# Optimization experiments

Hardware: AMD Instinct MI355X
Metric: run time of the kernel (lower is better)

Reference implementation:

```python
import jax, jax.numpy as jnp
import numpy as np

N_NODES = 100000
FEAT = 128
N_EDGES = 1600000


def setup_inputs() -> dict:
    key = jax.random.key(0)
    k1, k2, k3, k4, k5 = jax.random.split(key, 5)
    weight = jax.random.normal(k1, (N_NODES, FEAT), dtype=jnp.float32)
    cj = jax.random.uniform(k2, (N_NODES, 1), dtype=jnp.float32)
    ci = jax.random.uniform(k3, (N_NODES, 1), dtype=jnp.float32)
    src = jax.random.randint(k4, (N_EDGES,), 0, N_NODES, dtype=jnp.int32)
    dst = jax.random.randint(k5, (N_EDGES,), 0, N_NODES, dtype=jnp.int32)
    return {"weight": weight, "cj": cj, "ci": ci, "src": src, "dst": dst}


def reference(weight, cj, ci, src, dst):
    # feat = weight * dropout(cj); dropout_rate=0.0 -> identity
    feat = weight * cj                      # [N, F]
    msgs = feat[src]                        # [E, F] copy_src gather
    h = jax.ops.segment_sum(msgs, dst, num_segments=weight.shape[0])  # [N, F]
    return h * ci                           # dst-side normalize
```

## Files before the change

kernel.cpp:

```cpp
#include <hip/hip_runtime.h>
#include <hip/hip_bf16.h>

#define FEAT 128
#define BINW 128
#define BINSHIFT 7
#define MAXBIN 1024
#define CAP 4096
#define TB 8192

__device__ __forceinline__ unsigned short f2b(float f) {
    __hip_bfloat16 h = __float2bfloat16(f);
    return *reinterpret_cast<unsigned short*>(&h);
}
__device__ __forceinline__ float b2f_lo(unsigned u) {
    unsigned x = u << 16;
    float f;
    __builtin_memcpy(&f, &x, 4);
    return f;
}
__device__ __forceinline__ float b2f_hi(unsigned u) {
    unsigned x = u & 0xFFFF0000u;
    float f;
    __builtin_memcpy(&f, &x, 4);
    return f;
}
__device__ __forceinline__ unsigned int pack2(float lo, float hi) {
    return (unsigned int)f2b(lo) | ((unsigned int)f2b(hi) << 16);
}


__global__ void build_kernel(const float* __restrict__ weight,
                             const float* __restrict__ cj,
                             const int* __restrict__ src,
                             const int* __restrict__ dst,
                             unsigned short* __restrict__ feat16,
                             unsigned* __restrict__ pair,
                             int* __restrict__ binCursor,
                             int N, int E, int NBIN, int NTILE, int ipt) {
    __shared__ int h[MAXBIN];
    __shared__ int base_l[MAXBIN];
    int tile = blockIdx.x;

    int NC = N * (FEAT / 8);
    int cbase = tile * 256 * ipt;
    for (int j = 0; j < ipt; ++j) {
        int i = cbase + j * 256 + threadIdx.x;
        if (i < NC) {
            int row = i >> 4;
            int seg = i & 15;
            float c = cj[row];
            const float4* p = reinterpret_cast<const float4*>(
                weight + (size_t)row * FEAT + seg * 8);
            float4 a = p[0], b4 = p[1];
            uint4 o;
            o.x = pack2(a.x * c, a.y * c);
            o.y = pack2(a.z * c, a.w * c);
            o.z = pack2(b4.x * c, b4.y * c);
            o.w = pack2(b4.z * c, b4.w * c);
            *reinterpret_cast<uint4*>(feat16 + (size_t)i * 8) = o;
        }
    }

    if (tile >= NTILE) return;

    for (int b = threadIdx.x; b < NBIN; b += 256) h[b] = 0;
    __syncthreads();
    int e0 = tile * TB;
    #pragma unroll 4
    for (int i = 0; i < TB / 256; ++i) {
        int e = e0 + i * 256 + threadIdx.x;
        if (e < E) atomicAdd(&h[dst[e] >> BINSHIFT], 1);
    }
    __syncthreads();
    for (int b = threadIdx.x; b < NBIN; b += 256) {
        int c = h[b];
        int a = (c > 0) ? atomicAdd(&binCursor[b], c) : 0;
        base_l[b] = b * CAP + a;
        h[b] = 0;
    }
    __syncthreads();
    #pragma unroll 4
    for (int i = 0; i < TB / 256; ++i) {
        int e = e0 + i * 256 + threadIdx.x;
        if (e < E) {
            int d = dst[e];
            int b = d >> BINSHIFT;
            int pos = atomicAdd(&h[b], 1);
            int idx = base_l[b] + pos;
            if (idx < (b + 1) * CAP)
                pair[idx] = (unsigned)src[e] | ((unsigned)(d & (BINW - 1)) << 17);
        }
    }
}

__global__ void __launch_bounds__(512)
fine_sort_kernel(unsigned* __restrict__ pair,
                 const int* __restrict__ binCursor,
                 int2* __restrict__ nodeinfo,
                 int N) {
    __shared__ int cnt[BINW];
    __shared__ int sbase[BINW];
    __shared__ unsigned stage[CAP];
    int bin = blockIdx.x;
    int t = threadIdx.x;
    if (t < BINW) cnt[t] = 0;
    __syncthreads();
    int start = bin * CAP;
    int len = binCursor[bin];
    if (len > CAP) len = CAP;

    for (int k = t; k < len; k += 512) {
        unsigned p = pair[start + k];
        stage[k] = p;
        atomicAdd(&cnt[p >> 17], 1);
    }
    __syncthreads();
    int mine = (t < BINW) ? cnt[t] : 0;
    if (t < BINW) sbase[t] = mine;
    __syncthreads();
    for (int d = 1; d < BINW; d <<= 1) {
        int v = 0;
        if (t < BINW && t >= d) v = sbase[t - d];
        __syncthreads();
        if (t < BINW) sbase[t] += v;
        __syncthreads();
    }
    if (t < BINW) {
        int excl = sbase[t] - mine;
        int node = (bin << BINSHIFT) + t;
        if (node < N) nodeinfo[node] = make_int2(start + excl, mine);
        sbase[t] = start + excl;
        cnt[t] = 0;
    }
    __syncthreads();
    for (int k = t; k < len; k += 512) {
        unsigned p = stage[k];
        int ld = p >> 17;
        int pos = atomicAdd(&cnt[ld], 1);
        pair[sbase[ld] + pos] = p & 0x1FFFF;
    }
}

__global__ void gather_kernel(const unsigned short* __restrict__ feat16,
                              const float* __restrict__ ci,
                              const int2* __restrict__ nodeinfo,
                              const int* __restrict__ src_sorted,
                              float* __restrict__ out, int N) {
    int gt = blockIdx.x * blockDim.x + threadIdx.x;
    int node = gt >> 6;
    if (node >= N) return;
    int lane = gt & 63;
    int fi   = (lane & 15) << 3;
    int q    = lane >> 4;
    int2 ni  = nodeinfo[node];
    int start = ni.x;
    int end   = ni.x + ni.y;
    float acc[8] = {0.f, 0.f, 0.f, 0.f, 0.f, 0.f, 0.f, 0.f};
    #pragma unroll 4
    for (int k = start + q; k < end; k += 4) {
        int s = src_sorted[k];
        uint4 u = *reinterpret_cast<const uint4*>(feat16 + ((size_t)s << 7) + fi);
        acc[0] += b2f_lo(u.x); acc[1] += b2f_hi(u.x);
        acc[2] += b2f_lo(u.y); acc[3] += b2f_hi(u.y);
        acc[4] += b2f_lo(u.z); acc[5] += b2f_hi(u.z);
        acc[6] += b2f_lo(u.w); acc[7] += b2f_hi(u.w);
    }
    #pragma unroll
    for (int j = 0; j < 8; ++j) {
        acc[j] += __shfl_xor(acc[j], 16);
        acc[j] += __shfl_xor(acc[j], 32);
    }
    if (q == 0) {
        float c = ci[node];
        float4 v0 = make_float4(acc[0] * c, acc[1] * c, acc[2] * c, acc[3] * c);
        float4 v1 = make_float4(acc[4] * c, acc[5] * c, acc[6] * c, acc[7] * c);
        float* o = out + ((size_t)node << 7) + fi;
        *reinterpret_cast<float4*>(o)     = v0;
        *reinterpret_cast<float4*>(o + 4) = v1;
    }
}


__global__ void zero_ints_kernel(int* __restrict__ p, int n) {
    int i = blockIdx.x * blockDim.x + threadIdx.x;
    if (i < n) p[i] = 0;
}

__global__ void convert_hist_kernel(const float* __restrict__ weight,
                                    const float* __restrict__ cj,
                                    const int* __restrict__ dst,
                                    int* __restrict__ counts,
                                    unsigned short* __restrict__ feat16,
                                    int N, int E) {
    int i = blockIdx.x * blockDim.x + threadIdx.x;
    int NC = N * (FEAT / 8);
    if (i < NC) {
        int row = i >> 4;
        int seg = i & 15;
        float c = cj[row];
        const float4* p = reinterpret_cast<const float4*>(weight + (size_t)row * FEAT + seg * 8);
        float4 a = p[0], b = p[1];
        uint4 o;
        o.x = pack2(a.x * c, a.y * c);
        o.y = pack2(a.z * c, a.w * c);
        o.z = pack2(b.x * c, b.y * c);
        o.w = pack2(b.z * c, b.w * c);
        *reinterpret_cast<uint4*>(feat16 + (size_t)i * 8) = o;
    }
    if (i < E) atomicAdd(&counts[dst[i]], 1);
}

__global__ void block_sum_kernel(const int* __restrict__ counts, int* __restrict__ bsum, int N) {
    __shared__ int s[256];
    int i = blockIdx.x * 256 + threadIdx.x;
    s[threadIdx.x] = (i < N) ? counts[i] : 0;
    __syncthreads();
    for (int off = 128; off > 0; off >>= 1) {
        if (threadIdx.x < off) s[threadIdx.x] += s[threadIdx.x + off];
        __syncthreads();
    }
    if (threadIdx.x == 0) bsum[blockIdx.x] = s[0];
}

__global__ void scan_bsum_kernel(int* __restrict__ bsum, int nb) {
    __shared__ int s[512];
    int t = threadIdx.x;
    int mine = (t < nb) ? bsum[t] : 0;
    s[t] = mine;
    __syncthreads();
    for (int off = 1; off < 512; off <<= 1) {
        int v = (t >= off) ? s[t - off] : 0;
        __syncthreads();
        s[t] += v;
        __syncthreads();
    }
    if (t < nb) bsum[t] = s[t] - mine;
}

__global__ void scan_counts_kernel(const int* __restrict__ counts, const int* __restrict__ bsum,
                                   int* __restrict__ offsets, int* __restrict__ cursor,
                                   int N, int E) {
    __shared__ int s[256];
    int t = threadIdx.x;
    int i = blockIdx.x * 256 + t;
    int mine = (i < N) ? counts[i] : 0;
    s[t] = mine;
    __syncthreads();
    for (int off = 1; off < 256; off <<= 1) {
        int v = (t >= off) ? s[t - off] : 0;
        __syncthreads();
        s[t] += v;
        __syncthreads();
    }
    if (i < N) {
        int o = bsum[blockIdx.x] + s[t] - mine;
        offsets[i] = o;
        cursor[i] = o;
    }
    if (i == 0 && blockIdx.x == 0) offsets[N] = E;
}

__global__ void bucket_kernel(const int* __restrict__ src, const int* __restrict__ dst,
                              int* __restrict__ cursor,
                              int* __restrict__ src_sorted, int E) {
    int i = blockIdx.x * blockDim.x + threadIdx.x;
    if (i < E) {
        int pos = atomicAdd(&cursor[dst[i]], 1);
        src_sorted[pos] = src[i];
    }
}

__global__ void gather_mid_kernel(const unsigned short* __restrict__ feat16,
                                  const float* __restrict__ ci,
                                  const int* __restrict__ offsets,
                                  const int* __restrict__ src_sorted,
                                  float* __restrict__ out, int N) {
    int gt = blockIdx.x * blockDim.x + threadIdx.x;
    int node = gt >> 6;
    if (node >= N) return;
    int lane = gt & 63;
    int fi   = (lane & 15) << 3;
    int q    = lane >> 4;
    int start = offsets[node];
    int end   = offsets[node + 1];
    float acc[8] = {0.f, 0.f, 0.f, 0.f, 0.f, 0.f, 0.f, 0.f};
    #pragma unroll 4
    for (int k = start + q; k < end; k += 4) {
        int s = src_sorted[k];
        uint4 u = *reinterpret_cast<const uint4*>(feat16 + ((size_t)s << 7) + fi);
        acc[0] += b2f_lo(u.x); acc[1] += b2f_hi(u.x);
        acc[2] += b2f_lo(u.y); acc[3] += b2f_hi(u.y);
        acc[4] += b2f_lo(u.z); acc[5] += b2f_hi(u.z);
        acc[6] += b2f_lo(u.w); acc[7] += b2f_hi(u.w);
    }
    #pragma unroll
    for (int j = 0; j < 8; ++j) {
        acc[j] += __shfl_xor(acc[j], 16);
        acc[j] += __shfl_xor(acc[j], 32);
    }
    if (q == 0) {
        float c = ci[node];
        float4 v0 = make_float4(acc[0] * c, acc[1] * c, acc[2] * c, acc[3] * c);
        float4 v1 = make_float4(acc[4] * c, acc[5] * c, acc[6] * c, acc[7] * c);
        float* o = out + ((size_t)node << 7) + fi;
        *reinterpret_cast<float4*>(o)     = v0;
        *reinterpret_cast<float4*>(o + 4) = v1;
    }
}


__global__ void gcmc_zero_kernel(float4* __restrict__ out, int n4) {
    int i = blockIdx.x * blockDim.x + threadIdx.x;
    if (i < n4) out[i] = make_float4(0.f, 0.f, 0.f, 0.f);
}

__global__ void gcmc_scatter_kernel(const float* __restrict__ weight,
                                    const float* __restrict__ cj,
                                    const int* __restrict__ src,
                                    const int* __restrict__ dst,
                                    float* __restrict__ out,
                                    int n_edges) {
    int t = blockIdx.x * blockDim.x + threadIdx.x;
    int e = t >> 5;
    int f = (t & 31) << 2;
    if (e >= n_edges) return;
    int s = src[e];
    int d = dst[e];
    float c = cj[s];
    const float4 w = *reinterpret_cast<const float4*>(weight + (size_t)s * FEAT + f);
    float* o = out + (size_t)d * FEAT + f;
    unsafeAtomicAdd(o + 0, w.x * c);
    unsafeAtomicAdd(o + 1, w.y * c);
    unsafeAtomicAdd(o + 2, w.z * c);
    unsafeAtomicAdd(o + 3, w.w * c);
}

__global__ void gcmc_scale_kernel(float4* __restrict__ out,
                                  const float* __restrict__ ci, int n4) {
    int i = blockIdx.x * blockDim.x + threadIdx.x;
    if (i < n4) {
        float c = ci[i >> 5];
        float4 v = out[i];
        v.x *= c; v.y *= c; v.z *= c; v.w *= c;
        out[i] = v;
    }
}


static inline size_t align256(size_t x) { return (x + 255) & ~(size_t)255; }

extern "C" void kernel_launch(void* const* d_in, const int* in_sizes, int n_in,
                              void* d_out, int out_size, void* d_ws, size_t ws_size,
                              hipStream_t stream) {
    const float* weight = (const float*)d_in[0];
    const float* cj     = (const float*)d_in[1];
    const float* ci     = (const float*)d_in[2];
    const int*   src    = (const int*)d_in[3];
    const int*   dst    = (const int*)d_in[4];
    float* out = (float*)d_out;

    const int N = in_sizes[1];
    const int E = in_sizes[3];

    const int NBIN  = (N + BINW - 1) >> BINSHIFT;
    const int NTILE = (E + TB - 1) / TB;

    size_t o_feat = 0;
    size_t o_pair = align256(o_feat + (size_t)N * FEAT * 2);
    size_t o_cur  = align256(o_pair + (size_t)NBIN * CAP * 4);
    size_t o_ni   = align256(o_cur + (size_t)NBIN * 4);
    size_t need_new = o_ni + (size_t)N * 8;

    if (ws_size >= need_new && NBIN <= MAXBIN && N <= (1 << 17) &&
        (long)E <= (long)NBIN * (CAP / 2)) {
        char* ws = (char*)d_ws;
        unsigned short* feat16 = (unsigned short*)(ws + o_feat);
        unsigned* pair  = (unsigned*)(ws + o_pair);
        int* binCursor  = (int*)(ws + o_cur);
        int2* nodeinfo  = (int2*)(ws + o_ni);

        const int NC = N * (FEAT / 8);
        int G = (NC + 256 * 8 - 1) / (256 * 8);
        if (G < NTILE) G = NTILE;
        const int ipt = (NC + G * 256 - 1) / (G * 256);

        hipMemsetAsync(binCursor, 0, (size_t)NBIN * 4, stream);
        build_kernel<<<G, 256, 0, stream>>>(
            weight, cj, src, dst, feat16, pair, binCursor, N, E, NBIN, NTILE, ipt);
        fine_sort_kernel<<<NBIN, 512, 0, stream>>>(pair, binCursor, nodeinfo, N);
        long threads = (long)N * 64;
        gather_kernel<<<(int)((threads + 255) / 256), 256, 0, stream>>>(
            feat16, ci, nodeinfo, (const int*)pair, out, N);
        return;
    }

    const int NB = (N + 255) / 256;
    size_t m_off = 0;
    size_t m_cur = align256(m_off + (size_t)(N + 1) * 4);
    size_t m_bsm = align256(m_cur + (size_t)N * 4);
    size_t m_src = align256(m_bsm + 512 * 4);
    size_t m_ft  = align256(m_src + (size_t)E * 4);
    size_t need_mid = m_ft + (size_t)N * FEAT * 2;

    if (ws_size >= need_mid && NB <= 512) {
        char* ws = (char*)d_ws;
        int* offsets    = (int*)(ws + m_off);
        int* cursor     = (int*)(ws + m_cur);
        int* bsum       = (int*)(ws + m_bsm);
        int* src_sorted = (int*)(ws + m_src);
        unsigned short* feat16 = (unsigned short*)(ws + m_ft);

        zero_ints_kernel<<<NB, 256, 0, stream>>>(cursor, N);
        {
            long T = (long)N * (FEAT / 8);
            if ((long)E > T) T = E;
            convert_hist_kernel<<<(int)((T + 255) / 256), 256, 0, stream>>>(
                weight, cj, dst, cursor, feat16, N, E);
        }
        block_sum_kernel<<<NB, 256, 0, stream>>>(cursor, bsum, N);
        scan_bsum_kernel<<<1, 512, 0, stream>>>(bsum, NB);
        scan_counts_kernel<<<NB, 256, 0, stream>>>(cursor, bsum, offsets, cursor, N, E);
        bucket_kernel<<<(E + 255) / 256, 256, 0, stream>>>(src, dst, cursor, src_sorted, E);
        long threads = (long)N * 64;
        gather_mid_kernel<<<(int)((threads + 255) / 256), 256, 0, stream>>>(
            feat16, ci, offsets, src_sorted, out, N);
        return;
    }

    const int total = N * FEAT;
    const int n4 = total >> 2;
    gcmc_zero_kernel<<<(n4 + 255) / 256, 256, 0, stream>>>((float4*)out, n4);
    const long threads = (long)E * 32;
    gcmc_scatter_kernel<<<(int)((threads + 255) / 256), 256, 0, stream>>>(
        weight, cj, src, dst, out, E);
    gcmc_scale_kernel<<<(n4 + 255) / 256, 256, 0, stream>>>((float4*)out, ci, n4);
}
```

Before: 125.8 us.

## Split build kernel into separate binning and conversion blocks with 1024 threads

The fused build kernel used to have every block convert a slice of features and then, for the first NTILE blocks, also bin edges. Now binning blocks (the first NTILE) and feature-conversion blocks (the rest) are disjoint, and blocks use 1024 threads with a fixed four chunks per thread for conversion. The aim is to stop binning blocks from serialising behind conversion work and to reduce per-block overhead for the edge histogram. Larger blocks may lower occupancy flexibility and change the mix of load balance across CUs.

```diff
diff --git a/kernel.cpp b/kernel.cpp
--- a/kernel.cpp
+++ b/kernel.cpp
@@ -7,6 +7,7 @@
 #define MAXBIN 1024
 #define CAP 4096
 #define TB 8192
+#define BBS 1024
 
 __device__ __forceinline__ unsigned short f2b(float f) {
     __hip_bfloat16 h = __float2bfloat16(f);
@@ -29,59 +30,63 @@
 }
 
 
-__global__ void build_kernel(const float* __restrict__ weight,
-                             const float* __restrict__ cj,
-                             const int* __restrict__ src,
-                             const int* __restrict__ dst,
-                             unsigned short* __restrict__ feat16,
-                             unsigned* __restrict__ pair,
-                             int* __restrict__ binCursor,
-                             int N, int E, int NBIN, int NTILE, int ipt) {
+__global__ void __launch_bounds__(BBS)
+build_kernel(const float* __restrict__ weight,
+             const float* __restrict__ cj,
+             const int* __restrict__ src,
+             const int* __restrict__ dst,
+             unsigned short* __restrict__ feat16,
+             unsigned* __restrict__ pair,
+             int* __restrict__ binCursor,
+             int N, int E, int NBIN, int NTILE, int ipt) {
     __shared__ int h[MAXBIN];
     __shared__ int base_l[MAXBIN];
     int tile = blockIdx.x;
-
-    int NC = N * (FEAT / 8);
-    int cbase = tile * 256 * ipt;
-    for (int j = 0; j < ipt; ++j) {
-        int i = cbase + j * 256 + threadIdx.x;
-        if (i < NC) {
-            int row = i >> 4;
-            int seg = i & 15;
-            float c = cj[row];
-            const float4* p = reinterpret_cast<const float4*>(
-                weight + (size_t)row * FEAT + seg * 8);
-            float4 a = p[0], b4 = p[1];
-            uint4 o;
-            o.x = pack2(a.x * c, a.y * c);
-            o.y = pack2(a.z * c, a.w * c);
-            o.z = pack2(b4.x * c, b4.y * c);
-            o.w = pack2(b4.z * c, b4.w * c);
-            *reinterpret_cast<uint4*>(feat16 + (size_t)i * 8) = o;
+    int t = threadIdx.x;
+
+    if (tile >= NTILE) {
+        int NC = N * (FEAT / 8);
+        int cb = tile - NTILE;
+        int cbase = cb * BBS * ipt;
+        for (int j = 0; j < ipt; ++j) {
+            int i = cbase + j * BBS + t;
+            if (i < NC) {
+                int row = i >> 4;
+                int seg = i & 15;
+                float c = cj[row];
+                const float4* p = reinterpret_cast<const float4*>(
+                    weight + (size_t)row * FEAT + seg * 8);
+                float4 a = p[0], b4 = p[1];
+                uint4 o;
+                o.x = pack2(a.x * c, a.y * c);
+                o.y = pack2(a.z * c, a.w * c);
+                o.z = pack2(b4.x * c, b4.y * c);
+                o.w = pack2(b4.z * c, b4.w * c);
+                *reinterpret_cast<uint4*>(feat16 + (size_t)i * 8) = o;
+            }
         }
-    }
-
-    if (tile >= NTILE) return;
-
-    for (int b = threadIdx.x; b < NBIN; b += 256) h[b] = 0;
+        return;
+    }
+
+    for (int b = t; b < NBIN; b += BBS) h[b] = 0;
     __syncthreads();
     int e0 = tile * TB;
-    #pragma unroll 4
-    for (int i = 0; i < TB / 256; ++i) {
-        int e = e0 + i * 256 + threadIdx.x;
+    #pragma unroll
+    for (int i = 0; i < TB / BBS; ++i) {
+        int e = e0 + i * BBS + t;
         if (e < E) atomicAdd(&h[dst[e] >> BINSHIFT], 1);
     }
     __syncthreads();
-    for (int b = threadIdx.x; b < NBIN; b += 256) {
+    for (int b = t; b < NBIN; b += BBS) {
         int c = h[b];
         int a = (c > 0) ? atomicAdd(&binCursor[b], c) : 0;
         base_l[b] = b * CAP + a;
         h[b] = 0;
     }
     __syncthreads();
-    #pragma unroll 4
-    for (int i = 0; i < TB / 256; ++i) {
-        int e = e0 + i * 256 + threadIdx.x;
+    #pragma unroll
+    for (int i = 0; i < TB / BBS; ++i) {
+        int e = e0 + i * BBS + t;
         if (e < E) {
             int d = dst[e];
             int b = d >> BINSHIFT;
@@ -379,13 +384,12 @@
         int* binCursor  = (int*)(ws + o_cur);
         int2* nodeinfo  = (int2*)(ws + o_ni);
 
-        const int NC = N * (FEAT / 8);
-        int G = (NC + 256 * 8 - 1) / (256 * 8);
-        if (G < NTILE) G = NTILE;
-        const int ipt = (NC + G * 256 - 1) / (G * 256);
+        const int NC  = N * (FEAT / 8);
+        const int ipt = 4;
+        const int GC  = (NC + BBS * ipt - 1) / (BBS * ipt);
 
         hipMemsetAsync(binCursor, 0, (size_t)NBIN * 4, stream);
-        build_kernel<<<G, 256, 0, stream>>>(
+        build_kernel<<<NTILE + GC, BBS, 0, stream>>>(
             weight, cj, src, dst, feat16, pair, binCursor, N, E, NBIN, NTILE, ipt);
         fine_sort_kernel<<<NBIN, 512, 0, stream>>>(pair, binCursor, nodeinfo, N);
         long threads = (long)N * 64;
```

New measurement: 108.9 us. 1.16x faster.
